# Kernel tuning notes

Hardware: AMD Instinct MI355X
Metric: run time of the kernel (lower is better)

The kernel has to match this reference:

```python
import jax, jax.numpy as jnp
import numpy as np

N_NODES = 100000
N_EDGES = 1600000
D_IN = 128
CH = [128, 128]
N_GRAPHS = 256


def _glorot(key, shape):
    lim = float(np.sqrt(6.0 / (shape[0] + shape[1])))
    return jax.random.uniform(key, shape, jnp.float32, -lim, lim)


def setup_inputs() -> dict:
    key = jax.random.key(0)
    ks = jax.random.split(key, 12)
    x = jax.random.normal(ks[0], (N_NODES, D_IN), jnp.float32)
    edge_index = jax.random.randint(ks[1], (2, N_EDGES), 0, N_NODES, jnp.int64)
    batch = jnp.sort(jax.random.randint(ks[2], (N_NODES,), 0, N_GRAPHS, jnp.int64))
    W1 = _glorot(ks[3], (D_IN, CH[0]))
    b1 = jnp.zeros((CH[0],), jnp.float32)
    W2 = _glorot(ks[4], (CH[0], CH[1]))
    b2 = jnp.zeros((CH[1],), jnp.float32)
    Wm1 = _glorot(ks[5], (CH[1], 500)); bm1 = jnp.zeros((500,), jnp.float32)
    Wm2 = _glorot(ks[6], (500, 100));   bm2 = jnp.zeros((100,), jnp.float32)
    Wm3 = _glorot(ks[7], (100, 1));     bm3 = jnp.zeros((1,), jnp.float32)
    return {"x": x, "edge_index": edge_index, "batch": batch,
            "W1": W1, "b1": b1, "W2": W2, "b2": b2,
            "Wm1": Wm1, "bm1": bm1, "Wm2": Wm2, "bm2": bm2,
            "Wm3": Wm3, "bm3": bm3}


def gcn_conv(x, W, b, src, dst, n_nodes):
    # GCNConv with add_self_loops=True, symmetric normalization.
    h = x @ W  # [N, C]
    deg = jnp.zeros((n_nodes,), h.dtype).at[dst].add(1.0) + 1.0  # +1 self loop
    dinv = jax.lax.rsqrt(deg)  # deg >= 1
    norm = dinv[src] * dinv[dst]  # [E]
    agg = jnp.zeros_like(h).at[dst].add(h[src] * norm[:, None])
    agg = agg + h * (dinv * dinv)[:, None]  # self-loop term, norm = dinv[i]^2
    return agg + b


def global_mean_pool(x, batch, n_graphs):
    s = jax.ops.segment_sum(x, batch, num_segments=n_graphs)
    cnt = jax.ops.segment_sum(jnp.ones((x.shape[0],), x.dtype), batch, num_segments=n_graphs)
    return s / jnp.maximum(cnt, 1.0)[:, None]


def reference(x, edge_index, batch, W1, b1, W2, b2, Wm1, bm1, Wm2, bm2, Wm3, bm3):
    src, dst = edge_index[0], edge_index[1]
    h = jax.nn.relu(gcn_conv(x, W1, b1, src, dst, N_NODES))
    h = jax.nn.relu(gcn_conv(h, W2, b2, src, dst, N_NODES))
    g = global_mean_pool(h, batch, N_GRAPHS)  # [G, CH1]
    g = jax.nn.relu(g @ Wm1 + bm1)
    g = jax.nn.relu(g @ Wm2 + bm2)
    return g @ Wm3 + bm3  # [G, 1]
```

## Files before the change

kernel.cpp:

```cpp
#include <hip/hip_runtime.h>

#define CDIM 128
#define NGRAPH 256
#define BSH 7
#define BCAP 4096
#define NBLK 256

typedef unsigned short bf16_t;
typedef __attribute__((ext_vector_type(8))) short bf16x8;
typedef __attribute__((ext_vector_type(4))) float f32x4;

__device__ __forceinline__ float bflo(unsigned u) { return __uint_as_float(u << 16); }
__device__ __forceinline__ float bfhi(unsigned u) { return __uint_as_float(u & 0xffff0000u); }
__device__ __forceinline__ unsigned short f2bf(float f) {
  unsigned u = __float_as_uint(f);
  u += 0x7fffu + ((u >> 16) & 1u);
  return (unsigned short)(u >> 16);
}

__global__ __launch_bounds__(256) void k_wprep(const float* __restrict__ W1,
    const float* __restrict__ W2, bf16_t* __restrict__ Wtg1, bf16_t* __restrict__ Wtg2) {
  int i = blockIdx.x * 256 + threadIdx.x;
  int n = i >> 7, k = i & 127;
  Wtg1[n * 128 + k] = f2bf(W1[k * 128 + n]);
  Wtg2[n * 128 + k] = f2bf(W2[k * 128 + n]);
}

__global__ __launch_bounds__(1024) void k_phist(const int* __restrict__ dst,
    int* __restrict__ phist, int E, int NB) {
  __shared__ int hist[1024];
  int t = blockIdx.x, tid = threadIdx.x;
  for (int i = tid; i < NB; i += 1024) hist[i] = 0;
  __syncthreads();
  int tile = (E + NBLK - 1) / NBLK;
  int lo = t * tile;
  int hi = lo + tile; if (hi > E) hi = E;
  for (int i = lo + tid; i < hi; i += 1024) atomicAdd(&hist[dst[i] >> BSH], 1);
  __syncthreads();
  for (int i = tid; i < NB; i += 1024) phist[i * NBLK + t] = hist[i];
}

__global__ __launch_bounds__(256) void k_bscan(int* __restrict__ phist,
    int* __restrict__ btot) {
  __shared__ int wsum[4];
  int b = blockIdx.x;
  int tid = threadIdx.x, lane = tid & 63, wave = tid >> 6;
  int orig = phist[b * NBLK + tid];
  int v = orig;
#pragma unroll
  for (int ofs = 1; ofs < 64; ofs <<= 1) {
    int u = __shfl_up(v, ofs, 64);
    if (lane >= ofs) v += u;
  }
  if (lane == 63) wsum[wave] = v;
  __syncthreads();
  int add = 0;
#pragma unroll
  for (int w = 0; w < 3; w++) if (w < wave) add += wsum[w];
  int incl = v + add;
  phist[b * NBLK + tid] = incl - orig;
  if (tid == 255) btot[b] = incl;
}

__global__ __launch_bounds__(1024) void k_boff(const int* __restrict__ bsums,
    int* __restrict__ boffs, int G) {
  __shared__ int sh[1024];
  int tid = threadIdx.x;
  int v = (tid < G) ? bsums[tid] : 0;
  sh[tid] = v;
  __syncthreads();
  for (int ofs = 1; ofs < 1024; ofs <<= 1) {
    int u = (tid >= ofs) ? sh[tid - ofs] : 0;
    __syncthreads();
    sh[tid] += u;
    __syncthreads();
  }
  if (tid < G) boffs[tid] = sh[tid] - v;
  if (tid == G) boffs[G] = (G > 0) ? sh[G - 1] : 0;
}

__global__ __launch_bounds__(1024) void k_pscatter(const int* __restrict__ src,
    const int* __restrict__ dst, const int* __restrict__ phist,
    const int* __restrict__ bbase, unsigned* __restrict__ tmp, int E, int NB) {
  __shared__ int cur[1024];
  int t = blockIdx.x, tid = threadIdx.x;
  for (int i = tid; i < NB; i += 1024) cur[i] = bbase[i] + phist[i * NBLK + t];
  __syncthreads();
  int tile = (E + NBLK - 1) / NBLK;
  int lo = t * tile;
  int hi = lo + tile; if (hi > E) hi = E;
  for (int i = lo + tid; i < hi; i += 1024) {
    int d = dst[i];
    int p = atomicAdd(&cur[d >> BSH], 1);
    tmp[p] = (unsigned)src[i] | ((unsigned)(d & 127) << 20);
  }
}

__global__ __launch_bounds__(256) void k_csort2(const unsigned* __restrict__ tmp,
    const int* __restrict__ bbase, int* __restrict__ rowptr, float* __restrict__ dinv,
    int* __restrict__ col, int N, int NB, int E) {
  __shared__ int hist[128];
  __shared__ int sc[128];
  __shared__ int lcur[128];
  __shared__ unsigned buf[BCAP];
  int b = blockIdx.x;
  int n0 = b << BSH;
  int base = bbase[b];
  int cnt = bbase[b + 1] - base;
  int tid = threadIdx.x;
  if (tid < 128) hist[tid] = 0;
  __syncthreads();
  for (int i = tid; i < cnt; i += 256) atomicAdd(&hist[(tmp[base + i] >> 20) & 127], 1);
  __syncthreads();
  if (tid < 128) sc[tid] = hist[tid];
  __syncthreads();
  for (int ofs = 1; ofs < 128; ofs <<= 1) {
    int v = (tid < 128 && tid >= ofs) ? sc[tid - ofs] : 0;
    __syncthreads();
    if (tid < 128) sc[tid] += v;
    __syncthreads();
  }
  if (tid < 128) {
    int excl = sc[tid] - hist[tid];
    lcur[tid] = excl;
    int node = n0 + tid;
    if (node < N) {
      rowptr[node] = base + excl;
      dinv[node] = rsqrtf((float)hist[tid] + 1.0f);
    }
  }
  if (b == 0 && tid == 0) rowptr[N] = E;
  __syncthreads();
  if (cnt <= BCAP) {
    for (int i = tid; i < cnt; i += 256) {
      unsigned pk = tmp[base + i];
      int p = atomicAdd(&lcur[(pk >> 20) & 127], 1);
      buf[p] = pk & 0xFFFFFu;
    }
    __syncthreads();
    for (int i = tid; i < cnt; i += 256) col[base + i] = (int)buf[i];
  } else {
    for (int i = tid; i < cnt; i += 256) {
      unsigned pk = tmp[base + i];
      int p = atomicAdd(&lcur[(pk >> 20) & 127], 1);
      col[base + p] = (int)(pk & 0xFFFFFu);
    }
  }
}

#define WSTRIDE 136
template <int BF16IN>
__global__ __launch_bounds__(256) void k_gemm(const void* __restrict__ Ap,
    const bf16_t* __restrict__ Wtg, bf16_t* __restrict__ Co, int M) {
  __shared__ bf16_t Wt[128 * WSTRIDE];
  int tid = threadIdx.x;
  for (int c2 = tid; c2 < 2048; c2 += 256) {
    int n = c2 >> 4;
    int k8 = (c2 & 15) << 3;
    *(uint4*)&Wt[n * WSTRIDE + k8] = *(const uint4*)&Wtg[n * 128 + k8];
  }
  __syncthreads();

  int wave = tid >> 6;
  int lane = tid & 63;
  int m = lane & 15;
  int q = lane >> 4;
  int nstrips = (M + 63) >> 6;

  for (int s = blockIdx.x; s < nstrips; s += gridDim.x) {
    int rowA = s * 64 + wave * 16 + m;
    if (rowA > M - 1) rowA = M - 1;
    bf16x8 a[4];
#pragma unroll
    for (int c = 0; c < 4; c++) {
      if (BF16IN) {
        a[c] = *(const bf16x8*)((const bf16_t*)Ap + (size_t)rowA * CDIM + c * 32 + q * 8);
      } else {
        const float* ap = (const float*)Ap + (size_t)rowA * CDIM + c * 32 + q * 8;
        float4 f0 = *(const float4*)ap;
        float4 f1 = *(const float4*)(ap + 4);
        union { bf16x8 v; unsigned short u[8]; } ua;
        ua.u[0] = f2bf(f0.x); ua.u[1] = f2bf(f0.y); ua.u[2] = f2bf(f0.z); ua.u[3] = f2bf(f0.w);
        ua.u[4] = f2bf(f1.x); ua.u[5] = f2bf(f1.y); ua.u[6] = f2bf(f1.z); ua.u[7] = f2bf(f1.w);
        a[c] = ua.v;
      }
    }
#pragma unroll
    for (int t = 0; t < 8; t++) {
      f32x4 acc = {0.f, 0.f, 0.f, 0.f};
#pragma unroll
      for (int c = 0; c < 4; c++) {
        bf16x8 bv = *(const bf16x8*)&Wt[(t * 16 + m) * WSTRIDE + c * 32 + q * 8];
        acc = __builtin_amdgcn_mfma_f32_16x16x32_bf16(a[c], bv, acc, 0, 0, 0);
      }
#pragma unroll
      for (int r = 0; r < 4; r++) {
        int row = s * 64 + wave * 16 + q * 4 + r;
        if (row < M) Co[(size_t)row * CDIM + t * 16 + m] = f2bf(acc[r]);
      }
    }
  }
}

__global__ __launch_bounds__(256) void k_agg0(const bf16_t* __restrict__ t,
    const int* __restrict__ rowptr, const int* __restrict__ col,
    const float* __restrict__ dinv, const float* __restrict__ bias,
    bf16_t* __restrict__ out, int N) {
  int wave = threadIdx.x >> 6;
  int lane = threadIdx.x & 63;
  int node = blockIdx.x * 4 + wave;
  if (node >= N) return;
  int half = lane >> 5;
  int c = lane & 31;
  const uint2* tp = (const uint2*)t;
  float di = dinv[node];
  uint2 sv = tp[(size_t)node * 32 + c];
  float sw = (half == 0) ? di : 0.f;
  float a0 = bflo(sv.x) * sw, a1 = bfhi(sv.x) * sw;
  float a2 = bflo(sv.y) * sw, a3 = bfhi(sv.y) * sw;
  int beg = rowptr[node], end = rowptr[node + 1];
  for (int base = beg; base < end; base += 64) {
    int rem = end - base;
    int cnt = rem < 64 ? rem : 64;
    int sL = 0; float wL = 0.f;
    if (lane < cnt) { sL = col[base + lane]; wL = dinv[sL]; }
    for (int k = 0; k < cnt; k += 8) {
      int j0 = k + half, j1 = k + 2 + half, j2 = k + 4 + half, j3 = k + 6 + half;
      int s0 = __shfl(sL, j0, 64); float w0 = __shfl(wL, j0, 64);
      int s1 = __shfl(sL, j1, 64); float w1 = __shfl(wL, j1, 64);
      int s2 = __shfl(sL, j2, 64); float w2 = __shfl(wL, j2, 64);
      int s3 = __shfl(sL, j3, 64); float w3 = __shfl(wL, j3, 64);
      if (j0 >= cnt) { s0 = node; w0 = 0.f; }
      if (j1 >= cnt) { s1 = node; w1 = 0.f; }
      if (j2 >= cnt) { s2 = node; w2 = 0.f; }
      if (j3 >= cnt) { s3 = node; w3 = 0.f; }
      uint2 v0 = tp[(size_t)s0 * 32 + c];
      uint2 v1 = tp[(size_t)s1 * 32 + c];
      uint2 v2 = tp[(size_t)s2 * 32 + c];
      uint2 v3 = tp[(size_t)s3 * 32 + c];
      a0 = fmaf(bflo(v0.x), w0, a0); a1 = fmaf(bfhi(v0.x), w0, a1);
      a2 = fmaf(bflo(v0.y), w0, a2); a3 = fmaf(bfhi(v0.y), w0, a3);
      a0 = fmaf(bflo(v1.x), w1, a0); a1 = fmaf(bfhi(v1.x), w1, a1);
      a2 = fmaf(bflo(v1.y), w1, a2); a3 = fmaf(bfhi(v1.y), w1, a3);
      a0 = fmaf(bflo(v2.x), w2, a0); a1 = fmaf(bfhi(v2.x), w2, a1);
      a2 = fmaf(bflo(v2.y), w2, a2); a3 = fmaf(bfhi(v2.y), w2, a3);
      a0 = fmaf(bflo(v3.x), w3, a0); a1 = fmaf(bfhi(v3.x), w3, a1);
      a2 = fmaf(bflo(v3.y), w3, a2); a3 = fmaf(bfhi(v3.y), w3, a3);
    }
  }
  a0 += __shfl_xor(a0, 32, 64);
  a1 += __shfl_xor(a1, 32, 64);
  a2 += __shfl_xor(a2, 32, 64);
  a3 += __shfl_xor(a3, 32, 64);
  if (half == 0) {
    float4 bb = ((const float4*)bias)[c];
    float o0 = fmaxf(fmaf(di, a0, bb.x), 0.f);
    float o1 = fmaxf(fmaf(di, a1, bb.y), 0.f);
    float o2 = fmaxf(fmaf(di, a2, bb.z), 0.f);
    float o3 = fmaxf(fmaf(di, a3, bb.w), 0.f);
    uint2 o;
    o.x = ((unsigned)f2bf(o1) << 16) | f2bf(o0);
    o.y = ((unsigned)f2bf(o3) << 16) | f2bf(o2);
    ((uint2*)(out + (size_t)node * CDIM))[c] = o;
  }
}

__global__ __launch_bounds__(256) void k_aggp(const bf16_t* __restrict__ t,
    const int* __restrict__ rowptr, const int* __restrict__ col,
    const float* __restrict__ dinv, const float* __restrict__ bias,
    const int* __restrict__ batch, float* __restrict__ gsum, int N) {
  int wave = threadIdx.x >> 6;
  int lane = threadIdx.x & 63;
  int half = lane >> 5;
  int c = lane & 31;
  const uint2* tp = (const uint2*)t;
  float4 bb = ((const float4*)bias)[c];
  int n0 = (blockIdx.x * 4 + wave) * 16;
  if (n0 >= N) return;
  int nEnd = n0 + 16; if (nEnd > N) nEnd = N;
  float p0 = 0.f, p1 = 0.f, p2 = 0.f, p3 = 0.f;
  int curb = batch[n0];

  for (int node = n0; node < nEnd; node++) {
    float di = dinv[node];
    uint2 sv = tp[(size_t)node * 32 + c];
    float sw = (half == 0) ? di : 0.f;
    float a0 = bflo(sv.x) * sw, a1 = bfhi(sv.x) * sw;
    float a2 = bflo(sv.y) * sw, a3 = bfhi(sv.y) * sw;
    int beg = rowptr[node], end = rowptr[node + 1];
    for (int base = beg; base < end; base += 64) {
      int rem = end - base;
      int cnt = rem < 64 ? rem : 64;
      int sL = 0; float wL = 0.f;
      if (lane < cnt) { sL = col[base + lane]; wL = dinv[sL]; }
      for (int k = 0; k < cnt; k += 8) {
        int j0 = k + half, j1 = k + 2 + half, j2 = k + 4 + half, j3 = k + 6 + half;
        int s0 = __shfl(sL, j0, 64); float w0 = __shfl(wL, j0, 64);
        int s1 = __shfl(sL, j1, 64); float w1 = __shfl(wL, j1, 64);
        int s2 = __shfl(sL, j2, 64); float w2 = __shfl(wL, j2, 64);
        int s3 = __shfl(sL, j3, 64); float w3 = __shfl(wL, j3, 64);
        if (j0 >= cnt) { s0 = node; w0 = 0.f; }
        if (j1 >= cnt) { s1 = node; w1 = 0.f; }
        if (j2 >= cnt) { s2 = node; w2 = 0.f; }
        if (j3 >= cnt) { s3 = node; w3 = 0.f; }
        uint2 v0 = tp[(size_t)s0 * 32 + c];
        uint2 v1 = tp[(size_t)s1 * 32 + c];
        uint2 v2 = tp[(size_t)s2 * 32 + c];
        uint2 v3 = tp[(size_t)s3 * 32 + c];
        a0 = fmaf(bflo(v0.x), w0, a0); a1 = fmaf(bfhi(v0.x), w0, a1);
        a2 = fmaf(bflo(v0.y), w0, a2); a3 = fmaf(bfhi(v0.y), w0, a3);
        a0 = fmaf(bflo(v1.x), w1, a0); a1 = fmaf(bfhi(v1.x), w1, a1);
        a2 = fmaf(bflo(v1.y), w1, a2); a3 = fmaf(bfhi(v1.y), w1, a3);
        a0 = fmaf(bflo(v2.x), w2, a0); a1 = fmaf(bfhi(v2.x), w2, a1);
        a2 = fmaf(bflo(v2.y), w2, a2); a3 = fmaf(bfhi(v2.y), w2, a3);
        a0 = fmaf(bflo(v3.x), w3, a0); a1 = fmaf(bfhi(v3.x), w3, a1);
        a2 = fmaf(bflo(v3.y), w3, a2); a3 = fmaf(bfhi(v3.y), w3, a3);
      }
    }
    a0 += __shfl_xor(a0, 32, 64);
    a1 += __shfl_xor(a1, 32, 64);
    a2 += __shfl_xor(a2, 32, 64);
    a3 += __shfl_xor(a3, 32, 64);
    if (half == 0) {
      float o0 = fmaxf(fmaf(di, a0, bb.x), 0.f);
      float o1 = fmaxf(fmaf(di, a1, bb.y), 0.f);
      float o2 = fmaxf(fmaf(di, a2, bb.z), 0.f);
      float o3 = fmaxf(fmaf(di, a3, bb.w), 0.f);
      int b = batch[node];
      if (b != curb) {
        atomicAdd(&gsum[curb * CDIM + c * 4 + 0], p0);
        atomicAdd(&gsum[curb * CDIM + c * 4 + 1], p1);
        atomicAdd(&gsum[curb * CDIM + c * 4 + 2], p2);
        atomicAdd(&gsum[curb * CDIM + c * 4 + 3], p3);
        curb = b; p0 = p1 = p2 = p3 = 0.f;
      }
      p0 += __uint_as_float((unsigned)f2bf(o0) << 16);
      p1 += __uint_as_float((unsigned)f2bf(o1) << 16);
      p2 += __uint_as_float((unsigned)f2bf(o2) << 16);
      p3 += __uint_as_float((unsigned)f2bf(o3) << 16);
    }
  }
  if (half == 0) {
    atomicAdd(&gsum[curb * CDIM + c * 4 + 0], p0);
    atomicAdd(&gsum[curb * CDIM + c * 4 + 1], p1);
    atomicAdd(&gsum[curb * CDIM + c * 4 + 2], p2);
    atomicAdd(&gsum[curb * CDIM + c * 4 + 3], p3);
  }
}

__global__ __launch_bounds__(512) void k_mlp1(const float* __restrict__ g,
    const int* __restrict__ batch, int N,
    const float* __restrict__ W, const float* __restrict__ b, float* __restrict__ o) {
  __shared__ float gs[CDIM];
  int bi = blockIdx.x, tid = threadIdx.x;
  if (tid < CDIM) {
    int lo = 0, hi = N;
    while (lo < hi) { int mid = (lo + hi) >> 1; if (batch[mid] < bi) lo = mid + 1; else hi = mid; }
    int s = lo;
    lo = 0; hi = N;
    int key = bi + 1;
    while (lo < hi) { int mid = (lo + hi) >> 1; if (batch[mid] < key) lo = mid + 1; else hi = mid; }
    float inv = 1.f / fmaxf((float)(lo - s), 1.f);
    gs[tid] = g[bi * CDIM + tid] * inv;
  }
  __syncthreads();
  if (tid < 500) {
    float acc = b[tid];
#pragma unroll 4
    for (int k = 0; k < CDIM; k++) acc = fmaf(gs[k], W[k * 500 + tid], acc);
    o[bi * 500 + tid] = fmaxf(acc, 0.f);
  }
}

__global__ __launch_bounds__(128) void k_mlp23(const float* __restrict__ a,
    const float* __restrict__ W2m, const float* __restrict__ b2m,
    const float* __restrict__ w3, const float* __restrict__ b3,
    float* __restrict__ o) {
  __shared__ float as[500];
  __shared__ float m2s[100];
  int bi = blockIdx.x, tid = threadIdx.x;
  for (int k = tid; k < 500; k += 128) as[k] = a[bi * 500 + k];
  __syncthreads();
  if (tid < 100) {
    float acc = b2m[tid];
    for (int k = 0; k < 500; k++) acc = fmaf(as[k], W2m[k * 100 + tid], acc);
    m2s[tid] = fmaxf(acc, 0.f) * w3[tid];
  }
  __syncthreads();
  if (tid < 64) {
    float v = m2s[tid] + ((tid + 64 < 100) ? m2s[tid + 64] : 0.f);
#pragma unroll
    for (int ofs = 32; ofs > 0; ofs >>= 1) v += __shfl_down(v, ofs, 64);
    if (tid == 0) o[bi] = v + b3[0];
  }
}

static inline size_t align_up(size_t v) { return (v + 255) & ~(size_t)255; }

extern "C" void kernel_launch(void* const* d_in, const int* in_sizes, int n_in,
                              void* d_out, int out_size, void* d_ws, size_t ws_size,
                              hipStream_t stream) {
  const float* x   = (const float*)d_in[0];
  const int*   ei  = (const int*)d_in[1];
  const int*   bat = (const int*)d_in[2];
  const float* W1  = (const float*)d_in[3];
  const float* b1  = (const float*)d_in[4];
  const float* W2  = (const float*)d_in[5];
  const float* b2  = (const float*)d_in[6];
  const float* Wm1 = (const float*)d_in[7];
  const float* bm1 = (const float*)d_in[8];
  const float* Wm2 = (const float*)d_in[9];
  const float* bm2 = (const float*)d_in[10];
  const float* Wm3 = (const float*)d_in[11];
  const float* bm3 = (const float*)d_in[12];
  float* out = (float*)d_out;

  const int E = in_sizes[1] / 2;
  const int N = in_sizes[2];
  const int* src = ei;
  const int* dst = ei + E;
  const int NB = (N + 127) >> BSH;
  const int M  = NB * NBLK;

  char* p = (char*)d_ws;
  bf16_t* t    = (bf16_t*)p;   p += align_up((size_t)N * CDIM * 2);
  bf16_t* h    = (bf16_t*)p;   p += align_up((size_t)N * CDIM * 2);
  int* rowptr  = (int*)p;      p += align_up((size_t)(N + 1) * 4);
  int* colx    = (int*)p;      p += align_up((size_t)E * 4);
  unsigned* tmp= (unsigned*)p; p += align_up((size_t)E * 4);
  float* dinv  = (float*)p;    p += align_up((size_t)N * 4);
  int* phist   = (int*)p;      p += align_up((size_t)M * 4);
  int* btot    = (int*)p;      p += align_up((size_t)NB * 4);
  int* bbase   = (int*)p;      p += align_up((size_t)(NB + 1) * 4);
  bf16_t* Wtg1 = (bf16_t*)p;   p += align_up((size_t)CDIM * CDIM * 2);
  bf16_t* Wtg2 = (bf16_t*)p;   p += align_up((size_t)CDIM * CDIM * 2);
  float* gb    = (float*)p;    p += align_up((size_t)NGRAPH * CDIM * 4);
  float* m1    = (float*)p;    p += align_up((size_t)NGRAPH * 500 * 4);
  (void)ws_size; (void)n_in; (void)out_size;

  hipMemsetAsync(gb, 0, (size_t)NGRAPH * CDIM * 4, stream);

  k_wprep<<<64, 256, 0, stream>>>(W1, W2, Wtg1, Wtg2);
  k_phist<<<NBLK, 1024, 0, stream>>>(dst, phist, E, NB);
  k_bscan<<<NB, 256, 0, stream>>>(phist, btot);
  k_boff<<<1, 1024, 0, stream>>>(btot, bbase, NB);
  k_pscatter<<<NBLK, 1024, 0, stream>>>(src, dst, phist, bbase, tmp, E, NB);
  k_csort2<<<NB, 256, 0, stream>>>(tmp, bbase, rowptr, dinv, colx, N, NB, E);

  k_gemm<0><<<512, 256, 0, stream>>>(x, Wtg1, t, N);
  k_agg0<<<(N + 3) / 4, 256, 0, stream>>>(t, rowptr, colx, dinv, b1, h, N);
  k_gemm<1><<<512, 256, 0, stream>>>(h, Wtg2, t, N);
  int pwaves = (N + 15) / 16;
  k_aggp<<<(pwaves + 3) / 4, 256, 0, stream>>>(t, rowptr, colx, dinv, b2,
                                               bat, gb, N);

  k_mlp1<<<NGRAPH, 512, 0, stream>>>(gb, bat, N, Wm1, bm1, m1);
  k_mlp23<<<NGRAPH, 128, 0, stream>>>(m1, Wm2, bm2, Wm3, bm3, out);
}
```

Before: 349.3 us.

## Fuse CSR-build preprocessing into one cooperative kernel and merge MLP kernels

Replaces the memset and six separate preprocessing launches (weight prep, partial histogram, bucket scan, offset scan, scatter, bucket sort) with a single cooperative kernel that separates the phases with grid syncs. It also fuses the two MLP kernels into one so the 500-wide hidden layer stays in shared memory. It halves the nodes per wave in the pooled aggregation to add parallelism. The aim is to cut launch gaps and global round trips, at the cost of grid-wide barriers, a fixed 256-block grid that handles the per-bucket sort with fewer, larger blocks, and more pooling atomics.

New measurement: 502.0 us. 1.44x slower.

```diff
diff --git a/kernel.cpp b/kernel.cpp
--- a/kernel.cpp
+++ b/kernel.cpp
@@ -1,4 +1,6 @@
 #include <hip/hip_runtime.h>
+#include <hip/hip_cooperative_groups.h>
+namespace cg = cooperative_groups;
 
 #define CDIM 128
 #define NGRAPH 256
@@ -18,132 +20,132 @@
   return (unsigned short)(u >> 16);
 }
 
-__global__ __launch_bounds__(256) void k_wprep(const float* __restrict__ W1,
-    const float* __restrict__ W2, bf16_t* __restrict__ Wtg1, bf16_t* __restrict__ Wtg2) {
-  int i = blockIdx.x * 256 + threadIdx.x;
-  int n = i >> 7, k = i & 127;
-  Wtg1[n * 128 + k] = f2bf(W1[k * 128 + n]);
-  Wtg2[n * 128 + k] = f2bf(W2[k * 128 + n]);
-}
-
-__global__ __launch_bounds__(1024) void k_phist(const int* __restrict__ dst,
-    int* __restrict__ phist, int E, int NB) {
+__global__ __launch_bounds__(1024) void k_prep(
+    const float* __restrict__ W1, const float* __restrict__ W2,
+    bf16_t* __restrict__ Wtg1, bf16_t* __restrict__ Wtg2,
+    const int* __restrict__ src, const int* __restrict__ dst,
+    int* __restrict__ phist, int* __restrict__ btot, int* __restrict__ bbase,
+    unsigned* __restrict__ tmp, int* __restrict__ rowptr,
+    float* __restrict__ dinv, int* __restrict__ col,
+    float* __restrict__ gb, int E, int N, int NB) {
+  cg::grid_group grid = cg::this_grid();
   __shared__ int hist[1024];
-  int t = blockIdx.x, tid = threadIdx.x;
+  __shared__ int wsum2[4][4];
+  __shared__ int shist[128];
+  __shared__ int ssc[128];
+  __shared__ int lcur[128];
+  __shared__ unsigned buf[BCAP];
+  int blk = blockIdx.x, tid = threadIdx.x;
+  int gidx = blk * 1024 + tid;
+
+  if (gidx < 16384) {
+    int n = gidx >> 7, k = gidx & 127;
+    Wtg1[n * 128 + k] = f2bf(W1[k * 128 + n]);
+    Wtg2[n * 128 + k] = f2bf(W2[k * 128 + n]);
+  }
+  if (gidx < NGRAPH * CDIM) gb[gidx] = 0.f;
+
   for (int i = tid; i < NB; i += 1024) hist[i] = 0;
   __syncthreads();
   int tile = (E + NBLK - 1) / NBLK;
-  int lo = t * tile;
+  int lo = blk * tile;
   int hi = lo + tile; if (hi > E) hi = E;
   for (int i = lo + tid; i < hi; i += 1024) atomicAdd(&hist[dst[i] >> BSH], 1);
   __syncthreads();
-  for (int i = tid; i < NB; i += 1024) phist[i * NBLK + t] = hist[i];
-}
-
-__global__ __launch_bounds__(256) void k_bscan(int* __restrict__ phist,
-    int* __restrict__ btot) {
-  __shared__ int wsum[4];
-  int b = blockIdx.x;
-  int tid = threadIdx.x, lane = tid & 63, wave = tid >> 6;
-  int orig = phist[b * NBLK + tid];
-  int v = orig;
-#pragma unroll
-  for (int ofs = 1; ofs < 64; ofs <<= 1) {
-    int u = __shfl_up(v, ofs, 64);
-    if (lane >= ofs) v += u;
-  }
-  if (lane == 63) wsum[wave] = v;
-  __syncthreads();
-  int add = 0;
-#pragma unroll
-  for (int w = 0; w < 3; w++) if (w < wave) add += wsum[w];
-  int incl = v + add;
-  phist[b * NBLK + tid] = incl - orig;
-  if (tid == 255) btot[b] = incl;
-}
-
-__global__ __launch_bounds__(1024) void k_boff(const int* __restrict__ bsums,
-    int* __restrict__ boffs, int G) {
-  __shared__ int sh[1024];
-  int tid = threadIdx.x;
-  int v = (tid < G) ? bsums[tid] : 0;
-  sh[tid] = v;
-  __syncthreads();
-  for (int ofs = 1; ofs < 1024; ofs <<= 1) {
-    int u = (tid >= ofs) ? sh[tid - ofs] : 0;
-    __syncthreads();
-    sh[tid] += u;
-    __syncthreads();
-  }
-  if (tid < G) boffs[tid] = sh[tid] - v;
-  if (tid == G) boffs[G] = (G > 0) ? sh[G - 1] : 0;
-}
-
-__global__ __launch_bounds__(1024) void k_pscatter(const int* __restrict__ src,
-    const int* __restrict__ dst, const int* __restrict__ phist,
-    const int* __restrict__ bbase, unsigned* __restrict__ tmp, int E, int NB) {
-  __shared__ int cur[1024];
-  int t = blockIdx.x, tid = threadIdx.x;
-  for (int i = tid; i < NB; i += 1024) cur[i] = bbase[i] + phist[i * NBLK + t];
-  __syncthreads();
-  int tile = (E + NBLK - 1) / NBLK;
-  int lo = t * tile;
-  int hi = lo + tile; if (hi > E) hi = E;
+  for (int i = tid; i < NB; i += 1024) phist[i * NBLK + blk] = hist[i];
+  grid.sync();
+
+  {
+    int sub = tid >> 8;
+    int stid = tid & 255;
+    int slane = stid & 63, swave = stid >> 6;
+    int b2 = blk + 256 * sub;
+    int orig = (b2 < NB) ? phist[b2 * NBLK + stid] : 0;
+    int v = orig;
+#pragma unroll
+    for (int ofs = 1; ofs < 64; ofs <<= 1) {
+      int u = __shfl_up(v, ofs, 64);
+      if (slane >= ofs) v += u;
+    }
+    if (slane == 63) wsum2[sub][swave] = v;
+    __syncthreads();
+    int add = 0;
+#pragma unroll
+    for (int w = 0; w < 3; w++) if (w < swave) add += wsum2[sub][w];
+    int incl = v + add;
+    if (b2 < NB) {
+      phist[b2 * NBLK + stid] = incl - orig;
+      if (stid == 255) btot[b2] = incl;
+    }
+  }
+  grid.sync();
+
+  if (blk == 0) {
+    int v = (tid < NB) ? btot[tid] : 0;
+    hist[tid] = v;
+    __syncthreads();
+    for (int ofs = 1; ofs < 1024; ofs <<= 1) {
+      int u = (tid >= ofs) ? hist[tid - ofs] : 0;
+      __syncthreads();
+      hist[tid] += u;
+      __syncthreads();
+    }
+    if (tid < NB) bbase[tid] = hist[tid] - v;
+    if (tid == NB) bbase[NB] = hist[NB - 1];
+  }
+  grid.sync();
+
+  for (int i = tid; i < NB; i += 1024) hist[i] = bbase[i] + phist[i * NBLK + blk];
+  __syncthreads();
   for (int i = lo + tid; i < hi; i += 1024) {
     int d = dst[i];
-    int p = atomicAdd(&cur[d >> BSH], 1);
+    int p = atomicAdd(&hist[d >> BSH], 1);
     tmp[p] = (unsigned)src[i] | ((unsigned)(d & 127) << 20);
   }
-}
-
-__global__ __launch_bounds__(256) void k_csort2(const unsigned* __restrict__ tmp,
-    const int* __restrict__ bbase, int* __restrict__ rowptr, float* __restrict__ dinv,
-    int* __restrict__ col, int N, int NB, int E) {
-  __shared__ int hist[128];
-  __shared__ int sc[128];
-  __shared__ int lcur[128];
-  __shared__ unsigned buf[BCAP];
-  int b = blockIdx.x;
-  int n0 = b << BSH;
-  int base = bbase[b];
-  int cnt = bbase[b + 1] - base;
-  int tid = threadIdx.x;
-  if (tid < 128) hist[tid] = 0;
-  __syncthreads();
-  for (int i = tid; i < cnt; i += 256) atomicAdd(&hist[(tmp[base + i] >> 20) & 127], 1);
-  __syncthreads();
-  if (tid < 128) sc[tid] = hist[tid];
-  __syncthreads();
-  for (int ofs = 1; ofs < 128; ofs <<= 1) {
-    int v = (tid < 128 && tid >= ofs) ? sc[tid - ofs] : 0;
-    __syncthreads();
-    if (tid < 128) sc[tid] += v;
-    __syncthreads();
-  }
-  if (tid < 128) {
-    int excl = sc[tid] - hist[tid];
-    lcur[tid] = excl;
-    int node = n0 + tid;
-    if (node < N) {
-      rowptr[node] = base + excl;
-      dinv[node] = rsqrtf((float)hist[tid] + 1.0f);
-    }
-  }
-  if (b == 0 && tid == 0) rowptr[N] = E;
-  __syncthreads();
-  if (cnt <= BCAP) {
-    for (int i = tid; i < cnt; i += 256) {
-      unsigned pk = tmp[base + i];
-      int p = atomicAdd(&lcur[(pk >> 20) & 127], 1);
-      buf[p] = pk & 0xFFFFFu;
-    }
-    __syncthreads();
-    for (int i = tid; i < cnt; i += 256) col[base + i] = (int)buf[i];
-  } else {
-    for (int i = tid; i < cnt; i += 256) {
-      unsigned pk = tmp[base + i];
-      int p = atomicAdd(&lcur[(pk >> 20) & 127], 1);
-      col[base + p] = (int)(pk & 0xFFFFFu);
+  grid.sync();
+
+  if (blk == 0 && tid == 0) rowptr[N] = E;
+  for (int b = blk; b < NB; b += NBLK) {
+    __syncthreads();
+    int n0 = b << BSH;
+    int base = bbase[b];
+    int cnt = bbase[b + 1] - base;
+    if (tid < 128) shist[tid] = 0;
+    __syncthreads();
+    for (int i = tid; i < cnt; i += 1024) atomicAdd(&shist[(tmp[base + i] >> 20) & 127], 1);
+    __syncthreads();
+    if (tid < 128) ssc[tid] = shist[tid];
+    __syncthreads();
+    for (int ofs = 1; ofs < 128; ofs <<= 1) {
+      int v = (tid < 128 && tid >= ofs) ? ssc[tid - ofs] : 0;
+      __syncthreads();
+      if (tid < 128) ssc[tid] += v;
+      __syncthreads();
+    }
+    if (tid < 128) {
+      int excl = ssc[tid] - shist[tid];
+      lcur[tid] = excl;
+      int node = n0 + tid;
+      if (node < N) {
+        rowptr[node] = base + excl;
+        dinv[node] = rsqrtf((float)shist[tid] + 1.0f);
+      }
+    }
+    __syncthreads();
+    if (cnt <= BCAP) {
+      for (int i = tid; i < cnt; i += 1024) {
+        unsigned pk = tmp[base + i];
+        int p = atomicAdd(&lcur[(pk >> 20) & 127], 1);
+        buf[p] = pk & 0xFFFFFu;
+      }
+      __syncthreads();
+      for (int i = tid; i < cnt; i += 1024) col[base + i] = (int)buf[i];
+    } else {
+      for (int i = tid; i < cnt; i += 1024) {
+        unsigned pk = tmp[base + i];
+        int p = atomicAdd(&lcur[(pk >> 20) & 127], 1);
+        col[base + p] = (int)(pk & 0xFFFFFu);
+      }
     }
   }
 }
@@ -275,9 +277,9 @@
   int c = lane & 31;
   const uint2* tp = (const uint2*)t;
   float4 bb = ((const float4*)bias)[c];
-  int n0 = (blockIdx.x * 4 + wave) * 16;
+  int n0 = (blockIdx.x * 4 + wave) * 8;
   if (n0 >= N) return;
-  int nEnd = n0 + 16; if (nEnd > N) nEnd = N;
+  int nEnd = n0 + 8; if (nEnd > N) nEnd = N;
   float p0 = 0.f, p1 = 0.f, p2 = 0.f, p3 = 0.f;
   int curb = batch[n0];
 
@@ -348,10 +350,15 @@
   }
 }
 
-__global__ __launch_bounds__(512) void k_mlp1(const float* __restrict__ g,
+__global__ __launch_bounds__(512) void k_mlp(const float* __restrict__ g,
     const int* __restrict__ batch, int N,
-    const float* __restrict__ W, const float* __restrict__ b, float* __restrict__ o) {
+    const float* __restrict__ Wm1, const float* __restrict__ bm1,
+    const float* __restrict__ Wm2, const float* __restrict__ bm2,
+    const float* __restrict__ wm3, const float* __restrict__ bm3,
+    float* __restrict__ out) {
   __shared__ float gs[CDIM];
+  __shared__ float m1s[500];
+  __shared__ float m2s[100];
   int bi = blockIdx.x, tid = threadIdx.x;
   if (tid < CDIM) {
     int lo = 0, hi = N;
@@ -365,33 +372,23 @@
   }
   __syncthreads();
   if (tid < 500) {
-    float acc = b[tid];
+    float acc = bm1[tid];
 #pragma unroll 4
-    for (int k = 0; k < CDIM; k++) acc = fmaf(gs[k], W[k * 500 + tid], acc);
-    o[bi * 500 + tid] = fmaxf(acc, 0.f);
-  }
-}
-
-__global__ __launch_bounds__(128) void k_mlp23(const float* __restrict__ a,
-    const float* __restrict__ W2m, const float* __restrict__ b2m,
-    const float* __restrict__ w3, const float* __restrict__ b3,
-    float* __restrict__ o) {
-  __shared__ float as[500];
-  __shared__ float m2s[100];
-  int bi = blockIdx.x, tid = threadIdx.x;
-  for (int k = tid; k < 500; k += 128) as[k] = a[bi * 500 + k];
+    for (int k = 0; k < CDIM; k++) acc = fmaf(gs[k], Wm1[k * 500 + tid], acc);
+    m1s[tid] = fmaxf(acc, 0.f);
+  }
   __syncthreads();
   if (tid < 100) {
-    float acc = b2m[tid];
-    for (int k = 0; k < 500; k++) acc = fmaf(as[k], W2m[k * 100 + tid], acc);
-    m2s[tid] = fmaxf(acc, 0.f) * w3[tid];
+    float acc = bm2[tid];
+    for (int k = 0; k < 500; k++) acc = fmaf(m1s[k], Wm2[k * 100 + tid], acc);
+    m2s[tid] = fmaxf(acc, 0.f) * wm3[tid];
   }
   __syncthreads();
   if (tid < 64) {
     float v = m2s[tid] + ((tid + 64 < 100) ? m2s[tid + 64] : 0.f);
 #pragma unroll
     for (int ofs = 32; ofs > 0; ofs >>= 1) v += __shfl_down(v, ofs, 64);
-    if (tid == 0) o[bi] = v + b3[0];
+    if (tid == 0) out[bi] = v + bm3[0];
   }
 }
 
@@ -415,11 +412,11 @@
   const float* bm3 = (const float*)d_in[12];
   float* out = (float*)d_out;
 
-  const int E = in_sizes[1] / 2;
-  const int N = in_sizes[2];
+  int E = in_sizes[1] / 2;
+  int N = in_sizes[2];
   const int* src = ei;
   const int* dst = ei + E;
-  const int NB = (N + 127) >> BSH;
+  int NB = (N + 127) >> BSH;
   const int M  = NB * NBLK;
 
   char* p = (char*)d_ws;
@@ -435,25 +432,19 @@
   bf16_t* Wtg1 = (bf16_t*)p;   p += align_up((size_t)CDIM * CDIM * 2);
   bf16_t* Wtg2 = (bf16_t*)p;   p += align_up((size_t)CDIM * CDIM * 2);
   float* gb    = (float*)p;    p += align_up((size_t)NGRAPH * CDIM * 4);
-  float* m1    = (float*)p;    p += align_up((size_t)NGRAPH * 500 * 4);
   (void)ws_size; (void)n_in; (void)out_size;
 
-  hipMemsetAsync(gb, 0, (size_t)NGRAPH * CDIM * 4, stream);
-
-  k_wprep<<<64, 256, 0, stream>>>(W1, W2, Wtg1, Wtg2);
-  k_phist<<<NBLK, 1024, 0, stream>>>(dst, phist, E, NB);
-  k_bscan<<<NB, 256, 0, stream>>>(phist, btot);
-  k_boff<<<1, 1024, 0, stream>>>(btot, bbase, NB);
-  k_pscatter<<<NBLK, 1024, 0, stream>>>(src, dst, phist, bbase, tmp, E, NB);
-  k_csort2<<<NB, 256, 0, stream>>>(tmp, bbase, rowptr, dinv, colx, N, NB, E);
+  void* kargs[] = {(void*)&W1, (void*)&W2, (void*)&Wtg1, (void*)&Wtg2,
+                   (void*)&src, (void*)&dst, (void*)&phist, (void*)&btot,
+                   (void*)&bbase, (void*)&tmp, (void*)&rowptr, (void*)&dinv,
+                   (void*)&colx, (void*)&gb, (void*)&E, (void*)&N, (void*)&NB};
+  hipLaunchCooperativeKernel((void*)k_prep, dim3(NBLK), dim3(1024), kargs, 0, stream);
 
   k_gemm<0><<<512, 256, 0, stream>>>(x, Wtg1, t, N);
   k_agg0<<<(N + 3) / 4, 256, 0, stream>>>(t, rowptr, colx, dinv, b1, h, N);
   k_gemm<1><<<512, 256, 0, stream>>>(h, Wtg2, t, N);
-  int pwaves = (N + 15) / 16;
+  int pwaves = (N + 7) / 8;
   k_aggp<<<(pwaves + 3) / 4, 256, 0, stream>>>(t, rowptr, colx, dinv, b2,
                                                bat, gb, N);
-
-  k_mlp1<<<NGRAPH, 512, 0, stream>>>(gb, bat, N, Wm1, bm1, m1);
-  k_mlp23<<<NGRAPH, 128, 0, stream>>>(m1, Wm2, bm2, Wm3, bm3, out);
-}
+  k_mlp<<<NGRAPH, 512, 0, stream>>>(gb, bat, N, Wm1, bm1, Wm2, bm2, Wm3, bm3, out);
+}
```
